# Kernel tuning notes

Hardware: AMD Instinct MI355X
Metric: run time of the kernel (lower is better)

## Reference

```python
import jax, jax.numpy as jnp
import numpy as np
from jax import lax

B = 64


def _conv_bn_relu(x, w, cb, s, t):
    # 3x3 conv pad=1 (SAME), eval-mode BN folded to per-channel scale s / shift t, ReLU
    y = lax.conv_general_dilated(x, w, (1, 1), 'SAME',
                                 dimension_numbers=('NCHW', 'OIHW', 'NCHW'))
    y = y + cb[None, :, None, None]
    y = y * s[None, :, None, None] + t[None, :, None, None]
    return jax.nn.relu(y)


def _maxpool(x, k):
    return lax.reduce_window(x, -jnp.inf, lax.max, (1, 1, k, k), (1, 1, k, k), 'VALID')


def _tensor_dlt(H4PT, CornerA):
    # Batched version of the per-sample 8x8 DLT solve (faithful to the original row layout)
    U = CornerA[:, 0::2]            # [B,4]
    V = CornerA[:, 1::2]
    Ud = U + H4PT[:, 0::2]
    Vd = V + H4PT[:, 1::2]
    z = jnp.zeros_like(U)
    o = jnp.ones_like(U)
    r0 = jnp.stack([z, z, z, -U, V, -o, Vd * U, Vd * V], axis=-1)   # [B,4,8]
    r1 = jnp.stack([U, V, o, z, z, z, -Ud * U, -Ud * V], axis=-1)   # [B,4,8]
    A = jnp.stack([r0, r1], axis=2).reshape(U.shape[0], 8, 8)        # interleave rows per point
    bvec = jnp.stack([-Vd, Ud], axis=2).reshape(U.shape[0], 8)
    h = jnp.linalg.solve(A, bvec[..., None])[..., 0]                 # [B,8]
    H = jnp.concatenate([h, jnp.ones((U.shape[0], 1), h.dtype)], axis=1)
    return H.reshape(-1, 3, 3)


def _bilinear_sample(img, xs, ys):
    # img [Hs,Ws]; xs, ys [Ho,Wo]; zeros padding outside (grid_sample semantics)
    Hs, Ws = img.shape
    x0 = jnp.floor(xs)
    y0 = jnp.floor(ys)
    wx = xs - x0
    wy = ys - y0
    x0i = x0.astype(jnp.int32)
    y0i = y0.astype(jnp.int32)

    def gat(yi, xi):
        valid = (xi >= 0) & (xi < Ws) & (yi >= 0) & (yi < Hs)
        v = img[jnp.clip(yi, 0, Hs - 1), jnp.clip(xi, 0, Ws - 1)]
        return jnp.where(valid, v, jnp.zeros((), img.dtype))

    v00 = gat(y0i, x0i)
    v01 = gat(y0i, x0i + 1)
    v10 = gat(y0i + 1, x0i)
    v11 = gat(y0i + 1, x0i + 1)
    return (v00 * (1 - wx) * (1 - wy) + v01 * wx * (1 - wy)
            + v10 * (1 - wx) * wy + v11 * wx * wy)


def _warp_perspective(imgs, Hm, out_hw=(128, 128)):
    # dst(x,y) = src(H^{-1} [x,y,1]); align_corners=True pixel coordinates
    Ho, Wo = out_hw
    dt = imgs.dtype
    ys, xs = jnp.meshgrid(jnp.arange(Ho, dtype=dt), jnp.arange(Wo, dtype=dt), indexing='ij')
    grid = jnp.stack([xs, ys, jnp.ones_like(xs)], axis=-1)           # [Ho,Wo,3]
    Hinv = jnp.linalg.inv(Hm)                                        # [B,3,3]
    pts = jnp.einsum('bij,hwj->bhwi', Hinv, grid)                    # [B,Ho,Wo,3]
    xs_s = pts[..., 0] / pts[..., 2]
    ys_s = pts[..., 1] / pts[..., 2]
    out = jax.vmap(_bilinear_sample)(imgs, xs_s, ys_s)               # [B,Ho,Wo]
    return out[:, None]                                              # [B,1,Ho,Wo]


def setup_inputs() -> dict:
    key = jax.random.key(0)
    ks = jax.random.split(key, 64)
    d = {}
    d['TCropABatch'] = jax.random.uniform(ks[0], (B, 128, 128), jnp.float32)
    d['TI1Batch'] = jax.random.uniform(ks[1], (B, 2, 128, 128), jnp.float32)
    d['TImgABatch'] = jax.random.uniform(ks[2], (B, 240, 320), jnp.float32)
    # corners of a 128x128 quad inside the 240x320 image: (x,y) per corner, 8 values
    x0 = jax.random.uniform(ks[3], (B,), jnp.float32, 0.0, 192.0)
    y0 = jax.random.uniform(ks[4], (B,), jnp.float32, 0.0, 112.0)
    d['TCornerBatch'] = jnp.stack(
        [x0, y0, x0 + 127.0, y0, x0, y0 + 127.0, x0 + 127.0, y0 + 127.0], axis=1)
    chans = [(2, 64), (64, 64), (64, 64), (64, 64), (64, 128), (128, 128), (128, 128), (128, 128)]
    ki = 5
    for i, (ci, co) in enumerate(chans, start=1):
        fan = ci * 9
        d[f'w{i}'] = jax.random.normal(ks[ki], (co, ci, 3, 3), jnp.float32) * np.float32((2.0 / fan) ** 0.5)
        d[f'cb{i}'] = jnp.zeros((co,), jnp.float32)
        d[f's{i}'] = jnp.ones((co,), jnp.float32) + 0.01 * jax.random.normal(ks[ki + 1], (co,), jnp.float32)
        d[f't{i}'] = 0.01 * jax.random.normal(ks[ki + 2], (co,), jnp.float32)
        ki += 3
    d['fcw'] = jax.random.normal(ks[ki], (1024, 512), jnp.float32) * 0.02
    d['fcb'] = jnp.zeros((1024,), jnp.float32)
    d['f1w'] = jax.random.normal(ks[ki + 1], (8, 1024), jnp.float32) * 0.01
    d['f1b'] = jnp.zeros((8,), jnp.float32)
    return d


def reference(TCropABatch, TI1Batch, TImgABatch, TCornerBatch,
              w1, cb1, s1, t1, w2, cb2, s2, t2, w3, cb3, s3, t3, w4, cb4, s4, t4,
              w5, cb5, s5, t5, w6, cb6, s6, t6, w7, cb7, s7, t7, w8, cb8, s8, t8,
              fcw, fcb, f1w, f1b):
    ws = [w1, w2, w3, w4, w5, w6, w7, w8]
    cbs = [cb1, cb2, cb3, cb4, cb5, cb6, cb7, cb8]
    ss = [s1, s2, s3, s4, s5, s6, s7, s8]
    ts = [t1, t2, t3, t4, t5, t6, t7, t8]
    pools = [None, 2, None, 2, None, 2, None, 6]
    out = TI1Batch
    for i in range(8):
        out = _conv_bn_relu(out, ws[i], cbs[i], ss[i], ts[i])
        if pools[i] is not None:
            out = _maxpool(out, pools[i])
    out = out.reshape(out.shape[0], -1)                 # [B,512]
    out = jax.nn.relu(out @ fcw.T + fcb)                # dropout is eval-mode identity
    H4PT = out @ f1w.T + f1b                            # [B,8]
    Hm = _tensor_dlt(H4PT, TCornerBatch)                # [B,3,3]
    b_Pred = _warp_perspective(TImgABatch, Hm)          # [B,1,128,128]
    return b_Pred
```

## Files before the change

### kernel.cpp

```cpp
#include <hip/hip_runtime.h>
#include <math.h>

typedef __attribute__((ext_vector_type(4))) float f32x4;
typedef __attribute__((ext_vector_type(8))) short sh8;

__device__ __forceinline__ float bf2f(unsigned short u){
    union { unsigned int i; float f; } v; v.i = ((unsigned)u) << 16; return v.f;
}
__device__ __forceinline__ unsigned short f2bf(float f){
    union { float f; unsigned int i; } v; v.f = f;
    unsigned int x = v.i;
    x += 0x7fff + ((x >> 16) & 1);
    return (unsigned short)(x >> 16);
}

struct WTArgs {
    const float* src[7];
    unsigned short* hi[7];
    int cin[7];
    int start[8];
};

__global__ void wtrans_all(WTArgs a)
{
    int e = blockIdx.x * 256 + threadIdx.x;
    if (e >= a.start[7]) return;
    int l = 0;
    while (e >= a.start[l + 1]) l++;
    int eL = e - a.start[l];
    int CIN = a.cin[l];
    int tap = eL % 9, rest = eL / 9;
    int ci = rest % CIN, co = rest / CIN;
    int COUT = (a.start[l + 1] - a.start[l]) / (9 * CIN);
    a.hi[l][(tap * COUT + co) * CIN + ci] = f2bf(a.src[l][eL]);
}

__global__ __launch_bounds__(256) void conv1_kernel(
    const float* __restrict__ in, const float* __restrict__ w,
    const float* __restrict__ cb, const float* __restrict__ sc,
    const float* __restrict__ tb, unsigned short* __restrict__ out)
{
    __shared__ float s_w[18 * 64];
    __shared__ float s_in[2][18 * 20];

    const int tid = threadIdx.x;
    const int b = blockIdx.y;
    const int tile = blockIdx.x;
    const int ty = tile >> 3, tx = tile & 7;
    const int y0 = ty * 16, x0 = tx * 16;

    for (int idx = tid; idx < 1152; idx += 256) {
        int co = idx & 63, kk2 = idx >> 6;
        s_w[kk2 * 64 + co] = w[co * 18 + kk2];
    }
    for (int idx = tid; idx < 2 * 324; idx += 256) {
        int ci = idx / 324, rem = idx % 324;
        int r = rem / 18, c = rem % 18;
        int gy = y0 + r - 1, gx = x0 + c - 1;
        float v = 0.f;
        if (gy >= 0 && gy < 128 && gx >= 0 && gx < 128)
            v = in[((size_t)(b * 2 + ci) * 128 + gy) * 128 + gx];
        s_in[ci][r * 20 + c] = v;
    }
    __syncthreads();

    const int cog = tid >> 5;
    const int slot = tid & 31;
    const int sy = slot >> 2, sx = slot & 3;

    float p[2][4][6];
#pragma unroll
    for (int ci = 0; ci < 2; ci++)
#pragma unroll
        for (int r = 0; r < 4; r++)
#pragma unroll
            for (int c = 0; c < 6; c++)
                p[ci][r][c] = s_in[ci][(2 * sy + r) * 20 + 4 * sx + c];

    float acc[2][4][8];
#pragma unroll
    for (int r = 0; r < 2; r++)
#pragma unroll
        for (int c = 0; c < 4; c++)
#pragma unroll
            for (int o = 0; o < 8; o++) acc[r][c][o] = 0.f;

#pragma unroll
    for (int kk2 = 0; kk2 < 18; kk2++) {
        const int ci = kk2 / 9, k = kk2 % 9;
        const int ky = k / 3, kx = k % 3;
        float wv[8];
#pragma unroll
        for (int q = 0; q < 2; q++) {
            f32x4 w4 = *(const f32x4*)(&s_w[kk2 * 64 + cog * 8 + q * 4]);
#pragma unroll
            for (int z = 0; z < 4; z++) wv[q * 4 + z] = w4[z];
        }
#pragma unroll
        for (int r = 0; r < 2; r++)
#pragma unroll
            for (int c = 0; c < 4; c++) {
                float pv = p[ci][r + ky][c + kx];
#pragma unroll
                for (int o = 0; o < 8; o++) acc[r][c][o] += pv * wv[o];
            }
    }

    float bb[8], ss[8], tt[8];
#pragma unroll
    for (int o = 0; o < 8; o++) { bb[o] = cb[cog*8+o]; ss[o] = sc[cog*8+o]; tt[o] = tb[cog*8+o]; }
#pragma unroll
    for (int r = 0; r < 2; r++)
#pragma unroll
        for (int c = 0; c < 4; c++) {
            unsigned short ov[8];
#pragma unroll
            for (int o = 0; o < 8; o++)
                ov[o] = f2bf(fmaxf((acc[r][c][o] + bb[o]) * ss[o] + tt[o], 0.f));
            int py = y0 + 2 * sy + r, px = x0 + 4 * sx + c;
            *(sh8*)(out + ((size_t)(b * 128 + py) * 128 + px) * 64 + cog * 8) = *(sh8*)ov;
        }
}

template<int CIN, int COUT, int HI, int WI, int POOL, int TW, int NPG, int KSPLIT>
__global__ __launch_bounds__(NPG * 128, 4) void conv_mfma(
    const unsigned short* __restrict__ in,
    const unsigned short* __restrict__ wgt,
    const float* __restrict__ cb, const float* __restrict__ sc,
    const float* __restrict__ tb, void* __restrict__ outv)
{
    constexpr int THREADS = NPG * 128;
    constexpr int TH = (TW == 32) ? 2 * NPG : 4 * NPG;
    constexpr int HALW = TW + 2, HALH = TH + 2;
    constexpr int NPIX = HALW * HALH;
    constexpr int CHUNKS = CIN / 64;
    constexpr int TILESX = WI / TW;
    constexpr int HO = HI / POOL, WO = WI / POOL;
    constexpr int ST = 68;
    constexpr int NCOG = COUT / 64;
    constexpr int GPT = 512 / THREADS;
    constexpr int LOG_NPG = (NPG == 4) ? 2 : 1;

    __shared__ __align__(16) unsigned short lds_A[NPIX * ST];
    __shared__ __align__(16) unsigned short lds_W[2][4096];

    const int tid = threadIdx.x;
    const int lane = tid & 63;
    const int i = lane & 15, j = lane >> 4;
    const int wv = tid >> 6;
    const int pg = wv & (NPG - 1);
    const int cg = wv >> LOG_NPG;
    const int tile = blockIdx.x;
    const int ty = tile / TILESX, tx = tile % TILESX;
    const int y0 = ty * TH, x0 = tx * TW;
    const int cogrp = (NCOG == 1) ? 0 : (blockIdx.y & (NCOG - 1));
    const int kc = (KSPLIT == 2) ? (blockIdx.y >> (NCOG == 2 ? 1 : 0)) : 0;
    const int coBase = cogrp * 64;
    const int b = blockIdx.z;

    f32x4 acc[4][2];
#pragma unroll
    for (int pf = 0; pf < 4; pf++)
#pragma unroll
        for (int cf = 0; cf < 2; cf++) acc[pf][cf] = (f32x4){0.f, 0.f, 0.f, 0.f};

    sh8 rw[GPT];

    constexpr int NCH = (KSPLIT == 2) ? 1 : CHUNKS;
    for (int cc = 0; cc < NCH; cc++) {
        const int c = (KSPLIT == 2) ? kc : cc;
        if (cc) __syncthreads();

        for (int u = tid; u < NPIX * 8; u += THREADS) {
            int hp = u >> 3, c16 = u & 7;
            int hy = hp / HALW, hx = hp % HALW;
            int gy = y0 + hy - 1, gx = x0 + hx - 1;
            sh8 v = (sh8){0,0,0,0,0,0,0,0};
            if (gy >= 0 && gy < HI && gx >= 0 && gx < WI)
                v = *(const sh8*)(in + ((size_t)(b * HI + gy) * WI + gx) * CIN + c * 64 + c16 * 8);
            *(sh8*)(&lds_A[hp * ST + c16 * 8]) = v;
        }

        auto LOADW = [&](int tap) {
#pragma unroll
            for (int q = 0; q < GPT; q++) {
                int g = tid + q * THREADS;
                int slot = g & 7;
                int co = g >> 3;
                int gl = slot ^ (co & 7);
                rw[q] = *(const sh8*)(wgt + ((size_t)(tap * COUT + coBase + co)) * CIN
                                      + c * 64 + gl * 8);
            }
        };
        auto WRITEW = [&](int bi) {
#pragma unroll
            for (int q = 0; q < GPT; q++)
                *(sh8*)(&lds_W[bi][(tid + q * THREADS) * 8]) = rw[q];
        };

        LOADW(0); WRITEW(0);
        __syncthreads();

#pragma unroll
        for (int tap = 0; tap < 9; tap++) {
            if (tap < 8) LOADW(tap + 1);
            const int ky = tap / 3, kx = tap % 3;
            const int bi = tap & 1;
#pragma unroll
            for (int kk = 0; kk < 2; kk++) {
                sh8 aF[4], bF[2];
#pragma unroll
                for (int pf = 0; pf < 4; pf++) {
                    const int nf = pg * 4 + pf;
                    int hy2, hx2;
                    if (TW == 32) { hy2 = (nf >> 1) + ky; hx2 = (nf & 1) * 16 + i + kx; }
                    else          { hy2 = nf + ky;        hx2 = i + kx; }
                    aF[pf] = *(const sh8*)(&lds_A[(hy2 * HALW + hx2) * ST + kk * 32 + j * 8]);
                }
#pragma unroll
                for (int cf = 0; cf < 2; cf++) {
                    const int co_l = cg * 32 + cf * 16 + i;
                    const int phys = ((kk << 2) | j) ^ (co_l & 7);
                    bF[cf] = *(const sh8*)(&lds_W[bi][(co_l * 8 + phys) * 8]);
                }
                __builtin_amdgcn_s_setprio(1);
#pragma unroll
                for (int pf = 0; pf < 4; pf++)
#pragma unroll
                    for (int cf = 0; cf < 2; cf++)
                        acc[pf][cf] = __builtin_amdgcn_mfma_f32_16x16x32_bf16(
                            aF[pf], bF[cf], acc[pf][cf], 0, 0, 0);
                __builtin_amdgcn_s_setprio(0);
            }
            if (tap < 8) { WRITEW((tap + 1) & 1); __syncthreads(); }
        }
    }

    if constexpr (KSPLIT == 2) {
        float* po = (float*)outv + (size_t)kc * 64 * HO * WO * COUT;
#pragma unroll
        for (int cf = 0; cf < 2; cf++) {
            const int co = coBase + cg * 32 + cf * 16 + i;
#pragma unroll
            for (int pf = 0; pf < 4; pf++) {
                const int nf = pg * 4 + pf;
                int py, pxb;
                if (TW == 32) { py = nf >> 1; pxb = (nf & 1) * 16; }
                else          { py = nf;      pxb = 0; }
#pragma unroll
                for (int r = 0; r < 4; r++)
                    po[((size_t)(b * HO + y0 + py) * WO + x0 + pxb + j * 4 + r) * COUT + co] =
                        acc[pf][cf][r];
            }
        }
        return;
    }

    unsigned short* out = (unsigned short*)outv;
#pragma unroll
    for (int cf = 0; cf < 2; cf++) {
        const int co = coBase + cg * 32 + cf * 16 + i;
        const float b3 = cb[co], s3 = sc[co], t3 = tb[co];
        if (POOL == 1) {
#pragma unroll
            for (int pf = 0; pf < 4; pf++) {
                const int nf = pg * 4 + pf;
                int py, pxb;
                if (TW == 32) { py = nf >> 1; pxb = (nf & 1) * 16; }
                else          { py = nf;      pxb = 0; }
#pragma unroll
                for (int r = 0; r < 4; r++) {
                    float v = fmaxf((acc[pf][cf][r] + b3) * s3 + t3, 0.f);
                    out[((size_t)(b * HO + y0 + py) * WO + x0 + pxb + j * 4 + r) * COUT + co] = f2bf(v);
                }
            }
        } else if constexpr (POOL == 2 && TW == 32) {
#pragma unroll
            for (int h = 0; h < 2; h++) {
                const int pfA = h, pfB = 2 + h;
#pragma unroll
                for (int r2 = 0; r2 < 2; r2++) {
                    float vA0 = fmaxf((acc[pfA][cf][2*r2]   + b3) * s3 + t3, 0.f);
                    float vA1 = fmaxf((acc[pfA][cf][2*r2+1] + b3) * s3 + t3, 0.f);
                    float vB0 = fmaxf((acc[pfB][cf][2*r2]   + b3) * s3 + t3, 0.f);
                    float vB1 = fmaxf((acc[pfB][cf][2*r2+1] + b3) * s3 + t3, 0.f);
                    float v = fmaxf(fmaxf(vA0, vA1), fmaxf(vB0, vB1));
                    int pox = (x0 >> 1) + h * 8 + j * 2 + r2;
                    int poy = (y0 >> 1) + pg;
                    out[((size_t)(b * HO + poy) * WO + pox) * COUT + co] = f2bf(v);
                }
            }
        }
    }
}

__global__ void combine_k(const float* __restrict__ part, const float* __restrict__ cb,
                          const float* __restrict__ sc, const float* __restrict__ tb,
                          unsigned short* __restrict__ out)
{
    int e = blockIdx.x * 256 + threadIdx.x;
    int co = e & 127;
    float v = part[e] + part[e + 2097152];
    out[e] = f2bf(fmaxf((v + cb[co]) * sc[co] + tb[co], 0.f));
}

__global__ void pool6_kernel(const unsigned short* __restrict__ in, float* __restrict__ out)
{
    int t = blockIdx.x * 256 + threadIdx.x;
    if (t >= 64 * 128 * 4) return;
    int ox = t & 1, oy = (t >> 1) & 1, c = (t >> 2) & 127, b = t >> 9;
    const unsigned short* p = in + ((size_t)(b * 16 + oy * 6) * 16 + ox * 6) * 128 + c;
    float m = -INFINITY;
#pragma unroll
    for (int r = 0; r < 6; r++)
#pragma unroll
        for (int cc = 0; cc < 6; cc++) m = fmaxf(m, bf2f(p[(r * 16 + cc) * 128]));
    out[(size_t)b * 512 + c * 4 + oy * 2 + ox] = m;
}

__global__ void fc1_kernel(const float* __restrict__ flat, const float* __restrict__ fcw,
                           const float* __restrict__ fcb, float* __restrict__ out1)
{
    int b = blockIdx.y;
    int jj = blockIdx.x * 256 + threadIdx.x;
    const f32x4* f = (const f32x4*)(flat + (size_t)b * 512);
    const f32x4* w = (const f32x4*)(fcw + (size_t)jj * 512);
    float s = fcb[jj];
    for (int k = 0; k < 128; k++) {
        f32x4 a = f[k], ww = w[k];
        s += a[0]*ww[0] + a[1]*ww[1] + a[2]*ww[2] + a[3]*ww[3];
    }
    out1[(size_t)b * 1024 + jj] = fmaxf(s, 0.f);
}

__global__ void fc2_kernel(const float* __restrict__ out1, const float* __restrict__ f1w,
                           const float* __restrict__ f1b, float* __restrict__ h4pt)
{
    int b = blockIdx.x;
    int o = threadIdx.x >> 5, s2 = threadIdx.x & 31;
    const float* pa = out1 + (size_t)b * 1024;
    const float* pw = f1w + (size_t)o * 1024;
    float s = 0.f;
    for (int k = s2; k < 1024; k += 32) s += pa[k] * pw[k];
#pragma unroll
    for (int m = 16; m; m >>= 1) s += __shfl_xor(s, m);
    if (s2 == 0) h4pt[b * 8 + o] = s + f1b[o];
}

__global__ __launch_bounds__(512) void dlt_kernel(
    const float* __restrict__ h4pt, const float* __restrict__ corner,
    double* __restrict__ hinv)
{
    const int t = threadIdx.x;
    const int lane = t & 63;
    const int r = lane & 7;
    const int base = lane & ~7;
    const int b = (t >> 6) * 8 + (lane >> 3);

    const int jq = r >> 1;
    const double U  = (double)corner[b * 8 + 2 * jq];
    const double V  = (double)corner[b * 8 + 2 * jq + 1];
    const double Ud = U + (double)h4pt[b * 8 + 2 * jq];
    const double Vd = V + (double)h4pt[b * 8 + 2 * jq + 1];

    double Ar[9];
    if ((r & 1) == 0) {
        Ar[0] = 0;  Ar[1] = 0;  Ar[2] = 0;
        Ar[3] = -U; Ar[4] = V;  Ar[5] = -1;
        Ar[6] = Vd * U; Ar[7] = Vd * V; Ar[8] = -Vd;
    } else {
        Ar[0] = U;  Ar[1] = V;  Ar[2] = 1;
        Ar[3] = 0;  Ar[4] = 0;  Ar[5] = 0;
        Ar[6] = -Ud * U; Ar[7] = -Ud * V; Ar[8] = Ud;
    }

#pragma unroll
    for (int col = 0; col < 8; col++) {
        double val = (r >= col) ? fabs(Ar[col]) : -1.0;
        int idx = r;
#pragma unroll
        for (int m = 1; m < 8; m <<= 1) {
            double ov = __shfl_xor(val, m, 64);
            int oi = __shfl_xor(idx, m, 64);
            if (ov > val || (ov == val && oi < idx)) { val = ov; idx = oi; }
        }
        const int src = (r == col) ? idx : (r == idx) ? col : r;
#pragma unroll
        for (int k = 0; k < 9; k++) Ar[k] = __shfl(Ar[k], base + src, 64);
        double pr[9];
#pragma unroll
        for (int k = 0; k < 9; k++) pr[k] = __shfl(Ar[k], base + col, 64);
        if (r > col) {
            const double f = Ar[col] / pr[col];
#pragma unroll
            for (int k = 0; k < 9; k++) Ar[k] -= f * pr[k];
        }
    }

    double h[9];
    h[8] = 1.0;
#pragma unroll
    for (int col = 7; col >= 0; col--) {
        const double xc = __shfl(Ar[8] / Ar[col], base + col, 64);
        h[col] = xc;
        if (r < col) Ar[8] -= Ar[col] * xc;
    }

    const double a = h[0], bb = h[1], cq = h[2], d = h[3], e = h[4],
                 f = h[5], g = h[6], hh = h[7], iq = h[8];
    const double C0 = e * iq - f * hh, C1 = cq * hh - bb * iq, C2 = bb * f - cq * e;
    const double C3 = f * g - d * iq,  C4 = a * iq - cq * g,   C5 = cq * d - a * f;
    const double C6 = d * hh - e * g,  C7 = bb * g - a * hh,   C8 = a * e - bb * d;
    const double det = a * C0 + bb * C3 + cq * C6;
    const double idet = 1.0 / det;
    double my = (r == 0) ? C0 : (r == 1) ? C1 : (r == 2) ? C2 : (r == 3) ? C3
              : (r == 4) ? C4 : (r == 5) ? C5 : (r == 6) ? C6 : C7;
    double* o = hinv + b * 9;
    o[r] = my * idet;
    if (r == 0) o[8] = C8 * idet;
}

__global__ void warp_kernel(const float* __restrict__ img, const double* __restrict__ hinv,
                            float* __restrict__ out)
{
    int b = blockIdx.y;
    int pix = blockIdx.x * 256 + threadIdx.x;
    int y = pix >> 7, x = pix & 127;
    const double* h = hinv + b * 9;
    double X = (double)x, Y = (double)y;
    double p0 = h[0] * X + h[1] * Y + h[2];
    double p1 = h[3] * X + h[4] * Y + h[5];
    double p2 = h[6] * X + h[7] * Y + h[8];
    double xs = p0 / p2, ys = p1 / p2;
    double x0d = floor(xs), y0d = floor(ys);
    double wx = xs - x0d, wy = ys - y0d;
    int x0 = (int)x0d, y0 = (int)y0d;
    const float* im = img + (size_t)b * 240 * 320;
    auto gat = [&](int yi, int xi) -> double {
        bool valid = (xi >= 0) & (xi < 320) & (yi >= 0) & (yi < 240);
        int yc = yi < 0 ? 0 : (yi > 239 ? 239 : yi);
        int xc = xi < 0 ? 0 : (xi > 319 ? 319 : xi);
        double v = (double)im[yc * 320 + xc];
        return valid ? v : 0.0;
    };
    double v00 = gat(y0, x0),     v01 = gat(y0, x0 + 1);
    double v10 = gat(y0 + 1, x0), v11 = gat(y0 + 1, x0 + 1);
    double rr = v00 * (1 - wx) * (1 - wy) + v01 * wx * (1 - wy)
              + v10 * (1 - wx) * wy       + v11 * wx * wy;
    out[((size_t)b << 14) + pix] = (float)rr;
}

extern "C" void kernel_launch(void* const* d_in, const int* in_sizes, int n_in,
                              void* d_out, int out_size, void* d_ws, size_t ws_size,
                              hipStream_t stream)
{
    const float* TI1     = (const float*)d_in[1];
    const float* TImgA   = (const float*)d_in[2];
    const float* TCorner = (const float*)d_in[3];
    const float* w[8], *cbp[8], *sp[8], *tp[8];
    for (int l = 0; l < 8; l++) {
        w[l]   = (const float*)d_in[4 + 4 * l];
        cbp[l] = (const float*)d_in[5 + 4 * l];
        sp[l]  = (const float*)d_in[6 + 4 * l];
        tp[l]  = (const float*)d_in[7 + 4 * l];
    }
    const float* fcw = (const float*)d_in[36];
    const float* fcb = (const float*)d_in[37];
    const float* f1w = (const float*)d_in[38];
    const float* f1b = (const float*)d_in[39];

    char* base = (char*)d_ws;
    unsigned short* A1   = (unsigned short*)(base);
    unsigned short* B2   = (unsigned short*)(base + 134217728);
    unsigned short* whiA = (unsigned short*)(base + 167772160);
    float*  feat = (float*) (base + 167772160 + 1253376);
    float*  fc1o = feat + 64 * 512;
    float*  h4pt = fc1o + 64 * 1024;
    double* hinv = (double*)(h4pt + 512);
    float*  outp = (float*)d_out;

    float*          part7 = (float*)A1;
    unsigned short* c7out = (unsigned short*)(base + 134217728 + 8388608);
    float*          part8 = (float*)A1;
    unsigned short* c8out = (unsigned short*)(base + 134217728 + 16777216);

    const int CINS[7]  = {64, 64, 64, 64, 128, 128, 128};
    const int COUTS[7] = {64, 64, 64, 128, 128, 128, 128};
    int wofs[8]; wofs[0] = 0;
    for (int l = 0; l < 7; l++) wofs[l + 1] = wofs[l] + 9 * COUTS[l] * CINS[l];

    WTArgs wa;
    for (int l = 0; l < 7; l++) {
        wa.src[l] = w[l + 1];
        wa.hi[l] = whiA + wofs[l];
        wa.cin[l] = CINS[l];
        wa.start[l] = wofs[l];
    }
    wa.start[7] = wofs[7];
    wtrans_all<<<(wofs[7] + 255) / 256, 256, 0, stream>>>(wa);

    conv1_kernel<<<dim3(64, 64), 256, 0, stream>>>(
        TI1, w[0], cbp[0], sp[0], tp[0], A1);
    conv_mfma<64, 64, 128, 128, 2, 32, 4, 1><<<dim3(64, 1, 64), 512, 0, stream>>>(
        A1, whiA + wofs[0], cbp[1], sp[1], tp[1], B2);
    conv_mfma<64, 64, 64, 64, 1, 32, 4, 1><<<dim3(16, 1, 64), 512, 0, stream>>>(
        B2, whiA + wofs[1], cbp[2], sp[2], tp[2], A1);
    conv_mfma<64, 64, 64, 64, 2, 32, 4, 1><<<dim3(16, 1, 64), 512, 0, stream>>>(
        A1, whiA + wofs[2], cbp[3], sp[3], tp[3], B2);
    conv_mfma<64, 128, 32, 32, 1, 32, 4, 1><<<dim3(4, 2, 64), 512, 0, stream>>>(
        B2, whiA + wofs[3], cbp[4], sp[4], tp[4], A1);
    conv_mfma<128, 128, 32, 32, 2, 32, 4, 1><<<dim3(4, 2, 64), 512, 0, stream>>>(
        A1, whiA + wofs[4], cbp[5], sp[5], tp[5], B2);
    conv_mfma<128, 128, 16, 16, 1, 16, 2, 2><<<dim3(2, 4, 64), 256, 0, stream>>>(
        B2, whiA + wofs[5], cbp[6], sp[6], tp[6], part7);
    combine_k<<<8192, 256, 0, stream>>>(part7, cbp[6], sp[6], tp[6], c7out);
    conv_mfma<128, 128, 16, 16, 1, 16, 2, 2><<<dim3(2, 4, 64), 256, 0, stream>>>(
        c7out, whiA + wofs[6], cbp[7], sp[7], tp[7], part8);
    combine_k<<<8192, 256, 0, stream>>>(part8, cbp[7], sp[7], tp[7], c8out);

    pool6_kernel<<<128, 256, 0, stream>>>(c8out, feat);
    fc1_kernel<<<dim3(4, 64), 256, 0, stream>>>(feat, fcw, fcb, fc1o);
    fc2_kernel<<<64, 256, 0, stream>>>(fc1o, f1w, f1b, h4pt);
    dlt_kernel<<<1, 512, 0, stream>>>(h4pt, TCorner, hinv);
    warp_kernel<<<dim3(64, 64), 256, 0, stream>>>(TImgA, hinv, outp);
}
```

Before: 319.5 us.

## Deepen weight prefetch to two taps and load all fragments before MFMAs

```diff
diff --git a/kernel.cpp b/kernel.cpp
--- a/kernel.cpp
+++ b/kernel.cpp
@@ -164,12 +164,32 @@
 #pragma unroll
         for (int cf = 0; cf < 2; cf++) acc[pf][cf] = (f32x4){0.f, 0.f, 0.f, 0.f};
 
-    sh8 rw[GPT];
+    sh8 rwA[GPT], rwB[GPT];
+
+    auto LOADW = [&](sh8 (&dst)[GPT], int c, int tap) {
+#pragma unroll
+        for (int q = 0; q < GPT; q++) {
+            int g = tid + q * THREADS;
+            int slot = g & 7;
+            int co = g >> 3;
+            int gl = slot ^ (co & 7);
+            dst[q] = *(const sh8*)(wgt + ((size_t)(tap * COUT + coBase + co)) * CIN
+                                  + c * 64 + gl * 8);
+        }
+    };
+    auto WRITEW = [&](int bi, sh8 (&src)[GPT]) {
+#pragma unroll
+        for (int q = 0; q < GPT; q++)
+            *(sh8*)(&lds_W[bi][(tid + q * THREADS) * 8]) = src[q];
+    };
 
     constexpr int NCH = (KSPLIT == 2) ? 1 : CHUNKS;
     for (int cc = 0; cc < NCH; cc++) {
         const int c = (KSPLIT == 2) ? kc : cc;
-        if (cc) __syncthreads();
+        if (cc) {
+            asm volatile("s_waitcnt lgkmcnt(0)" ::: "memory");
+            __builtin_amdgcn_s_barrier();
+        }
 
         for (int u = tid; u < NPIX * 8; u += THREADS) {
             int hp = u >> 3, c16 = u & 7;
@@ -181,58 +201,77 @@
             *(sh8*)(&lds_A[hp * ST + c16 * 8]) = v;
         }
 
-        auto LOADW = [&](int tap) {
-#pragma unroll
-            for (int q = 0; q < GPT; q++) {
-                int g = tid + q * THREADS;
-                int slot = g & 7;
-                int co = g >> 3;
-                int gl = slot ^ (co & 7);
-                rw[q] = *(const sh8*)(wgt + ((size_t)(tap * COUT + coBase + co)) * CIN
-                                      + c * 64 + gl * 8);
-            }
-        };
-        auto WRITEW = [&](int bi) {
-#pragma unroll
-            for (int q = 0; q < GPT; q++)
-                *(sh8*)(&lds_W[bi][(tid + q * THREADS) * 8]) = rw[q];
-        };
-
-        LOADW(0); WRITEW(0);
-        __syncthreads();
+        LOADW(rwA, c, 0);
+        LOADW(rwB, c, 1);
+        WRITEW(0, rwA);
+        LOADW(rwA, c, 2);
+        asm volatile("s_waitcnt lgkmcnt(0)" ::: "memory");
+        __builtin_amdgcn_s_barrier();
 
 #pragma unroll
         for (int tap = 0; tap < 9; tap++) {
-            if (tap < 8) LOADW(tap + 1);
             const int ky = tap / 3, kx = tap % 3;
             const int bi = tap & 1;
+            if (tap < 8) {
+                if (bi == 0) WRITEW(1, rwB); else WRITEW(0, rwA);
+            }
+            if (tap <= 5) {
+                if (bi == 0) LOADW(rwB, c, tap + 3); else LOADW(rwA, c, tap + 3);
+            }
+            sh8 aF[4], bF[2];
 #pragma unroll
             for (int kk = 0; kk < 2; kk++) {
-                sh8 aF[4], bF[2];
 #pragma unroll
                 for (int pf = 0; pf < 4; pf++) {
-                    const int nf = pg * 4 + pf;
-                    int hy2, hx2;
-                    if (TW == 32) { hy2 = (nf >> 1) + ky; hx2 = (nf & 1) * 16 + i + kx; }
-                    else          { hy2 = nf + ky;        hx2 = i + kx; }
-                    aF[pf] = *(const sh8*)(&lds_A[(hy2 * HALW + hx2) * ST + kk * 32 + j * 8]);
+                    if (kk == 1) continue;
                 }
-#pragma unroll
-                for (int cf = 0; cf < 2; cf++) {
-                    const int co_l = cg * 32 + cf * 16 + i;
-                    const int phys = ((kk << 2) | j) ^ (co_l & 7);
-                    bF[cf] = *(const sh8*)(&lds_W[bi][(co_l * 8 + phys) * 8]);
-                }
-                __builtin_amdgcn_s_setprio(1);
-#pragma unroll
-                for (int pf = 0; pf < 4; pf++)
-#pragma unroll
-                    for (int cf = 0; cf < 2; cf++)
-                        acc[pf][cf] = __builtin_amdgcn_mfma_f32_16x16x32_bf16(
-                            aF[pf], bF[cf], acc[pf][cf], 0, 0, 0);
-                __builtin_amdgcn_s_setprio(0);
-            }
-            if (tap < 8) { WRITEW((tap + 1) & 1); __syncthreads(); }
+            }
+#pragma unroll
+            for (int pf = 0; pf < 4; pf++) {
+                const int nf = pg * 4 + pf;
+                int hy2, hx2;
+                if (TW == 32) { hy2 = (nf >> 1) + ky; hx2 = (nf & 1) * 16 + i + kx; }
+                else          { hy2 = nf + ky;        hx2 = i + kx; }
+                aF[pf] = *(const sh8*)(&lds_A[(hy2 * HALW + hx2) * ST + 0 * 32 + j * 8]);
+            }
+#pragma unroll
+            for (int cf = 0; cf < 2; cf++) {
+                const int co_l = cg * 32 + cf * 16 + i;
+                const int phys = ((0 << 2) | j) ^ (co_l & 7);
+                bF[cf] = *(const sh8*)(&lds_W[bi][(co_l * 8 + phys) * 8]);
+            }
+            sh8 aF2[4], bF2[2];
+#pragma unroll
+            for (int pf = 0; pf < 4; pf++) {
+                const int nf = pg * 4 + pf;
+                int hy2, hx2;
+                if (TW == 32) { hy2 = (nf >> 1) + ky; hx2 = (nf & 1) * 16 + i + kx; }
+                else          { hy2 = nf + ky;        hx2 = i + kx; }
+                aF2[pf] = *(const sh8*)(&lds_A[(hy2 * HALW + hx2) * ST + 1 * 32 + j * 8]);
+            }
+#pragma unroll
+            for (int cf = 0; cf < 2; cf++) {
+                const int co_l = cg * 32 + cf * 16 + i;
+                const int phys = ((1 << 2) | j) ^ (co_l & 7);
+                bF2[cf] = *(const sh8*)(&lds_W[bi][(co_l * 8 + phys) * 8]);
+            }
+            asm volatile("s_waitcnt lgkmcnt(0)" ::: "memory");
+            if (tap < 8 || cc + 1 < NCH) __builtin_amdgcn_s_barrier();
+
+            __builtin_amdgcn_s_setprio(1);
+#pragma unroll
+            for (int pf = 0; pf < 4; pf++)
+#pragma unroll
+                for (int cf = 0; cf < 2; cf++)
+                    acc[pf][cf] = __builtin_amdgcn_mfma_f32_16x16x32_bf16(
+                        aF[pf], bF[cf], acc[pf][cf], 0, 0, 0);
+#pragma unroll
+            for (int pf = 0; pf < 4; pf++)
+#pragma unroll
+                for (int cf = 0; cf < 2; cf++)
+                    acc[pf][cf] = __builtin_amdgcn_mfma_f32_16x16x32_bf16(
+                        aF2[pf], bF2[cf], acc[pf][cf], 0, 0, 0);
+            __builtin_amdgcn_s_setprio(0);
         }
     }
 
```

Result: slower. 328.1 us (+2.7%).

## Add 4-wave conv kernel with 64-channel per-wave output tiles for layers 2-6

Applied to the files above, without the earlier changes.

```diff
diff --git a/kernel.cpp b/kernel.cpp
--- a/kernel.cpp
+++ b/kernel.cpp
@@ -120,6 +120,154 @@
             int py = y0 + 2 * sy + r, px = x0 + 4 * sx + c;
             *(sh8*)(out + ((size_t)(b * 128 + py) * 128 + px) * 64 + cog * 8) = *(sh8*)ov;
         }
+}
+
+template<int CIN, int COUT, int HI, int WI, int POOL, int TW>
+__global__ __launch_bounds__(256, 2) void conv_v4(
+    const unsigned short* __restrict__ in,
+    const unsigned short* __restrict__ wgt,
+    const float* __restrict__ cb, const float* __restrict__ sc,
+    const float* __restrict__ tb, unsigned short* __restrict__ out)
+{
+    constexpr int TH = 256 / TW;
+    constexpr int HALW = TW + 2, HALH = TH + 2;
+    constexpr int NPIX = HALW * HALH;
+    constexpr int CHUNKS = CIN / 64;
+    constexpr int TILESX = WI / TW;
+    constexpr int HO = HI / POOL, WO = WI / POOL;
+    constexpr int ST = 68;
+
+    __shared__ __align__(16) unsigned short lds_A[NPIX * ST];
+    __shared__ __align__(16) unsigned short lds_W[2][4096];
+
+    const int tid = threadIdx.x;
+    const int lane = tid & 63;
+    const int i = lane & 15, j = lane >> 4;
+    const int wv = tid >> 6;
+    const int tile = blockIdx.x;
+    const int ty = tile / TILESX, tx = tile % TILESX;
+    const int y0 = ty * TH, x0 = tx * TW;
+    const int coBase = blockIdx.y * 64;
+    const int b = blockIdx.z;
+
+    const int co_s = tid >> 2;
+    const int gp = tid & 3;
+
+    f32x4 acc[4][4];
+#pragma unroll
+    for (int pf = 0; pf < 4; pf++)
+#pragma unroll
+        for (int cf = 0; cf < 4; cf++) acc[pf][cf] = (f32x4){0.f, 0.f, 0.f, 0.f};
+
+    sh8 rw[2];
+
+    for (int c = 0; c < CHUNKS; c++) {
+        if (c) __syncthreads();
+
+        for (int u = tid; u < NPIX * 8; u += 256) {
+            int hp = u >> 3, c16 = u & 7;
+            int hy = hp / HALW, hx = hp % HALW;
+            int gy = y0 + hy - 1, gx = x0 + hx - 1;
+            sh8 v = (sh8){0,0,0,0,0,0,0,0};
+            if (gy >= 0 && gy < HI && gx >= 0 && gx < WI)
+                v = *(const sh8*)(in + ((size_t)(b * HI + gy) * WI + gx) * CIN + c * 64 + c16 * 8);
+            *(sh8*)(&lds_A[hp * ST + c16 * 8]) = v;
+        }
+
+        const unsigned short* wrow = wgt + ((size_t)(coBase + co_s)) * CIN + c * 64;
+
+        auto LOADW = [&](int tap) {
+#pragma unroll
+            for (int q = 0; q < 2; q++) {
+                int pp = gp + q * 4;
+                int gl = pp ^ (co_s & 7);
+                rw[q] = *(const sh8*)(wrow + (size_t)tap * COUT * CIN + gl * 8);
+            }
+        };
+        auto WRITEW = [&](int bi) {
+#pragma unroll
+            for (int q = 0; q < 2; q++) {
+                int pp = gp + q * 4;
+                *(sh8*)(&lds_W[bi][co_s * 64 + pp * 8]) = rw[q];
+            }
+        };
+
+        LOADW(0); WRITEW(0);
+        __syncthreads();
+
+#pragma unroll
+        for (int tap = 0; tap < 9; tap++) {
+            if (tap < 8) LOADW(tap + 1);
+            const int ky = tap / 3, kx = tap % 3;
+            const int bi = tap & 1;
+            sh8 aF[8], bF[8];
+#pragma unroll
+            for (int kk = 0; kk < 2; kk++) {
+#pragma unroll
+                for (int pf = 0; pf < 4; pf++) {
+                    const int nf = wv * 4 + pf;
+                    int hy2, hx2;
+                    if (TW == 32) { hy2 = (nf >> 1) + ky; hx2 = (nf & 1) * 16 + i + kx; }
+                    else          { hy2 = nf + ky;        hx2 = i + kx; }
+                    aF[kk * 4 + pf] = *(const sh8*)(&lds_A[(hy2 * HALW + hx2) * ST + kk * 32 + j * 8]);
+                }
+#pragma unroll
+                for (int cf = 0; cf < 4; cf++) {
+                    const int co_l = cf * 16 + i;
+                    bF[kk * 4 + cf] = *(const sh8*)(&lds_W[bi][co_l * 64
+                        + ((((kk << 2) | j) ^ (i & 7)) * 8)]);
+                }
+            }
+            __builtin_amdgcn_s_setprio(1);
+#pragma unroll
+            for (int kk = 0; kk < 2; kk++)
+#pragma unroll
+                for (int pf = 0; pf < 4; pf++)
+#pragma unroll
+                    for (int cf = 0; cf < 4; cf++)
+                        acc[pf][cf] = __builtin_amdgcn_mfma_f32_16x16x32_bf16(
+                            aF[kk * 4 + pf], bF[kk * 4 + cf], acc[pf][cf], 0, 0, 0);
+            __builtin_amdgcn_s_setprio(0);
+            if (tap < 8) { WRITEW((tap + 1) & 1); __syncthreads(); }
+        }
+    }
+
+#pragma unroll
+    for (int cf = 0; cf < 4; cf++) {
+        const int co = coBase + cf * 16 + i;
+        const float b3 = cb[co], s3 = sc[co], t3 = tb[co];
+        if (POOL == 1) {
+#pragma unroll
+            for (int pf = 0; pf < 4; pf++) {
+                const int nf = wv * 4 + pf;
+                int py, pxb;
+                if (TW == 32) { py = nf >> 1; pxb = (nf & 1) * 16; }
+                else          { py = nf;      pxb = 0; }
+#pragma unroll
+                for (int r = 0; r < 4; r++) {
+                    float v = fmaxf((acc[pf][cf][r] + b3) * s3 + t3, 0.f);
+                    int px = pxb + j * 4 + r;
+                    out[((size_t)(b * HO + y0 + py) * WO + x0 + px) * COUT + co] = f2bf(v);
+                }
+            }
+        } else if constexpr (POOL == 2 && TW == 32) {
+#pragma unroll
+            for (int h = 0; h < 2; h++) {
+                const int pfA = h, pfB = 2 + h;
+#pragma unroll
+                for (int r2 = 0; r2 < 2; r2++) {
+                    float vA0 = fmaxf((acc[pfA][cf][2*r2]   + b3) * s3 + t3, 0.f);
+                    float vA1 = fmaxf((acc[pfA][cf][2*r2+1] + b3) * s3 + t3, 0.f);
+                    float vB0 = fmaxf((acc[pfB][cf][2*r2]   + b3) * s3 + t3, 0.f);
+                    float vB1 = fmaxf((acc[pfB][cf][2*r2+1] + b3) * s3 + t3, 0.f);
+                    float v = fmaxf(fmaxf(vA0, vA1), fmaxf(vB0, vB1));
+                    int pox = (x0 >> 1) + h * 8 + j * 2 + r2;
+                    int poy = (y0 >> 1) + wv;
+                    out[((size_t)(b * HO + poy) * WO + pox) * COUT + co] = f2bf(v);
+                }
+            }
+        }
+    }
 }
 
 template<int CIN, int COUT, int HI, int WI, int POOL, int TW, int NPG, int KSPLIT>
@@ -142,7 +290,7 @@
     constexpr int LOG_NPG = (NPG == 4) ? 2 : 1;
 
     __shared__ __align__(16) unsigned short lds_A[NPIX * ST];
-    __shared__ __align__(16) unsigned short lds_W[2][4096];
+    __shared__ __align__(16) unsigned short lds_W[2 * 4096];
 
     const int tid = threadIdx.x;
     const int lane = tid & 63;
@@ -195,7 +343,7 @@
         auto WRITEW = [&](int bi) {
 #pragma unroll
             for (int q = 0; q < GPT; q++)
-                *(sh8*)(&lds_W[bi][(tid + q * THREADS) * 8]) = rw[q];
+                *(sh8*)(&lds_W[bi * 4096 + (tid + q * THREADS) * 8]) = rw[q];
         };
 
         LOADW(0); WRITEW(0);
@@ -221,7 +369,7 @@
                 for (int cf = 0; cf < 2; cf++) {
                     const int co_l = cg * 32 + cf * 16 + i;
                     const int phys = ((kk << 2) | j) ^ (co_l & 7);
-                    bF[cf] = *(const sh8*)(&lds_W[bi][(co_l * 8 + phys) * 8]);
+                    bF[cf] = *(const sh8*)(&lds_W[bi * 4096 + co_l * 64 + phys * 8]);
                 }
                 __builtin_amdgcn_s_setprio(1);
 #pragma unroll
@@ -272,22 +420,6 @@
                 for (int r = 0; r < 4; r++) {
                     float v = fmaxf((acc[pf][cf][r] + b3) * s3 + t3, 0.f);
                     out[((size_t)(b * HO + y0 + py) * WO + x0 + pxb + j * 4 + r) * COUT + co] = f2bf(v);
-                }
-            }
-        } else if constexpr (POOL == 2 && TW == 32) {
-#pragma unroll
-            for (int h = 0; h < 2; h++) {
-                const int pfA = h, pfB = 2 + h;
-#pragma unroll
-                for (int r2 = 0; r2 < 2; r2++) {
-                    float vA0 = fmaxf((acc[pfA][cf][2*r2]   + b3) * s3 + t3, 0.f);
-                    float vA1 = fmaxf((acc[pfA][cf][2*r2+1] + b3) * s3 + t3, 0.f);
-                    float vB0 = fmaxf((acc[pfB][cf][2*r2]   + b3) * s3 + t3, 0.f);
-                    float vB1 = fmaxf((acc[pfB][cf][2*r2+1] + b3) * s3 + t3, 0.f);
-                    float v = fmaxf(fmaxf(vA0, vA1), fmaxf(vB0, vB1));
-                    int pox = (x0 >> 1) + h * 8 + j * 2 + r2;
-                    int poy = (y0 >> 1) + pg;
-                    out[((size_t)(b * HO + poy) * WO + pox) * COUT + co] = f2bf(v);
                 }
             }
         }
@@ -501,15 +633,15 @@
 
     conv1_kernel<<<dim3(64, 64), 256, 0, stream>>>(
         TI1, w[0], cbp[0], sp[0], tp[0], A1);
-    conv_mfma<64, 64, 128, 128, 2, 32, 4, 1><<<dim3(64, 1, 64), 512, 0, stream>>>(
+    conv_v4<64, 64, 128, 128, 2, 32><<<dim3(64, 1, 64), 256, 0, stream>>>(
         A1, whiA + wofs[0], cbp[1], sp[1], tp[1], B2);
-    conv_mfma<64, 64, 64, 64, 1, 32, 4, 1><<<dim3(16, 1, 64), 512, 0, stream>>>(
+    conv_v4<64, 64, 64, 64, 1, 32><<<dim3(16, 1, 64), 256, 0, stream>>>(
         B2, whiA + wofs[1], cbp[2], sp[2], tp[2], A1);
-    conv_mfma<64, 64, 64, 64, 2, 32, 4, 1><<<dim3(16, 1, 64), 512, 0, stream>>>(
+    conv_v4<64, 64, 64, 64, 2, 32><<<dim3(16, 1, 64), 256, 0, stream>>>(
         A1, whiA + wofs[2], cbp[3], sp[3], tp[3], B2);
-    conv_mfma<64, 128, 32, 32, 1, 32, 4, 1><<<dim3(4, 2, 64), 512, 0, stream>>>(
+    conv_v4<64, 128, 32, 32, 1, 32><<<dim3(4, 2, 64), 256, 0, stream>>>(
         B2, whiA + wofs[3], cbp[4], sp[4], tp[4], A1);
-    conv_mfma<128, 128, 32, 32, 2, 32, 4, 1><<<dim3(4, 2, 64), 512, 0, stream>>>(
+    conv_v4<128, 128, 32, 32, 2, 32><<<dim3(4, 2, 64), 256, 0, stream>>>(
         A1, whiA + wofs[4], cbp[5], sp[5], tp[5], B2);
     conv_mfma<128, 128, 16, 16, 1, 16, 2, 2><<<dim3(2, 4, 64), 256, 0, stream>>>(
         B2, whiA + wofs[5], cbp[6], sp[6], tp[6], part7);
```

Measured after the change: 343.2 us. 7.4% more time.
